# Performance work log

Hardware: AMD Instinct MI355X
Metric: run time of the kernel (lower is better)

Reference implementation:

```python
import jax, jax.numpy as jnp
import numpy as np

N_NODES = 100000
N_EDGES = 3200000
IN_CH = 32
HID = 16


def setup_inputs() -> dict:
    key = jax.random.key(0)
    ks = jax.random.split(key, 8)
    x = jax.random.normal(ks[0], (N_NODES, IN_CH), dtype=jnp.float32)
    edge_index = jax.random.randint(ks[1], (2, N_EDGES), 0, N_NODES, dtype=jnp.int64)
    s1 = 1.0 / np.sqrt(IN_CH)
    s2 = 1.0 / np.sqrt(HID)
    Wl1 = jax.random.normal(ks[2], (HID, IN_CH), dtype=jnp.float32) * s1
    Wr1 = jax.random.normal(ks[3], (HID, IN_CH), dtype=jnp.float32) * s1
    b1 = jnp.zeros((HID,), dtype=jnp.float32)
    Wl2 = jax.random.normal(ks[4], (1, HID), dtype=jnp.float32) * s2
    Wr2 = jax.random.normal(ks[5], (1, HID), dtype=jnp.float32) * s2
    b2 = jnp.zeros((1,), dtype=jnp.float32)
    return {"x": x, "edge_index": edge_index, "Wl1": Wl1, "Wr1": Wr1,
            "b1": b1, "Wl2": Wl2, "Wr2": Wr2, "b2": b2}


def _sage_conv(h, src, dst, deg_inv, Wl, Wr, b):
    # mean aggregation of source features at destination nodes
    msg_sum = jax.ops.segment_sum(h[src], dst, num_segments=N_NODES)  # [N, F]
    agg = msg_sum * deg_inv[:, None]
    # lin_l(agg) + lin_r(h): lin_l carries the bias (PyG SAGEConv convention)
    return agg @ Wl.T + b + h @ Wr.T


def reference(x, edge_index, Wl1, Wr1, b1, Wl2, Wr2, b2):
    src = edge_index[0]
    dst = edge_index[1]
    deg = jax.ops.segment_sum(jnp.ones((N_EDGES,), dtype=x.dtype), dst,
                              num_segments=N_NODES)
    deg_inv = 1.0 / jnp.maximum(deg, 1.0)  # mean; nodes w/o in-edges get 0 agg

    h = _sage_conv(x, src, dst, deg_inv, Wl1, Wr1, b1)
    h = jax.nn.relu(h)
    # F.dropout in eval mode -> identity
    out = _sage_conv(h, src, dst, deg_inv, Wl2, Wr2, b2)
    return out.squeeze(-1)  # [N]
```

## Files before the change

kernel.cpp:

```cpp
#include <hip/hip_runtime.h>

#define N_NODES 100000
#define N_EDGES 3200000
#define NB_F 782
#define RSZ 4992
#define TILE 6250
#define NTILES 512
#define PRJ_BLOCKS 196
#define MAXIT 13
#define MAXB 10


__device__ __forceinline__ float bf2f_lo(unsigned int w) {
  return __uint_as_float(w << 16);
}
__device__ __forceinline__ float bf2f_hi(unsigned int w) {
  return __uint_as_float(w & 0xFFFF0000u);
}
__device__ __forceinline__ unsigned short f2bf(float f) {
  unsigned int b = __float_as_uint(f);
  return (unsigned short)((b + 0x7FFFu + ((b >> 16) & 1u)) >> 16);
}

__global__ __launch_bounds__(512) void k_front(
    const int* __restrict__ ei, const float* __restrict__ x,
    const float* __restrict__ Wl1, const float* __restrict__ Wr1,
    const float* __restrict__ b1, int* __restrict__ gcur,
    int* __restrict__ recs, unsigned short* __restrict__ p1h,
    float* __restrict__ q1b) {
  __shared__ int smem[11693];
  const int t = threadIdx.x;

  if (blockIdx.x < PRJ_BLOCKS) {
    float* sWl = (float*)smem;
    float* sWr = (float*)smem + 512;
    float* sb  = (float*)smem + 1024;
    sWl[t] = Wl1[t];
    sWr[t] = Wr1[t];
    if (t < 16) sb[t] = b1[t];
    __syncthreads();

    const int n = blockIdx.x * 512 + t;
    if (n >= N_NODES) return;

    float xr[32];
    const float4* xp = (const float4*)(x + (size_t)n * 32);
#pragma unroll
    for (int j = 0; j < 8; ++j) {
      float4 v = xp[j];
      xr[4 * j + 0] = v.x;
      xr[4 * j + 1] = v.y;
      xr[4 * j + 2] = v.z;
      xr[4 * j + 3] = v.w;
    }
    float pv[16], qv[16];
#pragma unroll
    for (int hh = 0; hh < 16; ++hh) {
      float a = 0.f, b = 0.f;
#pragma unroll
      for (int i = 0; i < 32; ++i) {
        a = fmaf(xr[i], sWl[hh * 32 + i], a);
        b = fmaf(xr[i], sWr[hh * 32 + i], b);
      }
      pv[hh] = a;
      qv[hh] = b + sb[hh];
    }
    unsigned int w[8];
#pragma unroll
    for (int j = 0; j < 8; ++j)
      w[j] = (unsigned int)f2bf(pv[2 * j]) |
             ((unsigned int)f2bf(pv[2 * j + 1]) << 16);
    uint4* pp = (uint4*)(p1h + (size_t)n * 16);
    pp[0] = make_uint4(w[0], w[1], w[2], w[3]);
    pp[1] = make_uint4(w[4], w[5], w[6], w[7]);
    float4* qp = (float4*)(q1b + (size_t)n * 16);
#pragma unroll
    for (int j = 0; j < 4; ++j)
      qp[j] =
          make_float4(qv[4 * j], qv[4 * j + 1], qv[4 * j + 2], qv[4 * j + 3]);
    return;
  }

  int* hist   = smem;
  int* delta  = smem + 1024;
  int* seg    = smem + 1806;
  int* stage  = smem + 2318;
  unsigned short* bid = (unsigned short*)(smem + 8568);
  for (int i = t; i < 1024; i += 512) hist[i] = 0;
  __syncthreads();

  const int tb = (blockIdx.x - PRJ_BLOCKS) * TILE;
  int rec[MAXIT], aux[MAXIT];
#pragma unroll
  for (int i = 0; i < MAXIT; ++i) {
    const int pos = t + i * 512;
    if (pos < TILE) {
      const int e = tb + pos;
      const int s = ei[e];
      const int d = ei[N_EDGES + e];
      const int k = d >> 7;
      const int rank = atomicAdd(&hist[k], 1);
      rec[i] = ((d & 127) << 17) | s;
      aux[i] = (k << 16) | rank;
    } else {
      aux[i] = -1;
    }
  }
  __syncthreads();

  const int s0 = hist[2 * t], s1 = hist[2 * t + 1];
  const int my = s0 + s1;
  seg[t] = my;
  __syncthreads();
#pragma unroll
  for (int o = 1; o < 512; o <<= 1) {
    const int a = (t >= o) ? seg[t - o] : 0;
    __syncthreads();
    seg[t] += a;
    __syncthreads();
  }
  const int ex = seg[t] - my;
  hist[2 * t] = ex;
  hist[2 * t + 1] = ex + s0;
  {
    const int b = 2 * t;
    if (b < NB_F && s0)
      delta[b] = b * RSZ + atomicAdd(&gcur[b * 16], s0) - ex;
    if (b + 1 < NB_F && s1)
      delta[b + 1] =
          (b + 1) * RSZ + atomicAdd(&gcur[(b + 1) * 16], s1) - (ex + s0);
  }
  __syncthreads();

#pragma unroll
  for (int i = 0; i < MAXIT; ++i) {
    if (aux[i] >= 0) {
      const int k = aux[i] >> 16;
      const int rank = aux[i] & 0xFFFF;
      stage[hist[k] + rank] = rec[i];
    }
  }
  for (int k2 = t; k2 < NB_F; k2 += 512) {
    const int st = hist[k2];
    const int en = hist[k2 + 1];
    for (int p = st; p < en; ++p) bid[p] = (unsigned short)k2;
  }
  __syncthreads();

  for (int pos = t; pos < TILE; pos += 512) {
    const int k = bid[pos];
    const int idx = delta[k] + pos;
    if ((unsigned)idx < (unsigned)(NB_F * RSZ)) recs[idx] = stage[pos];
  }
}

__global__ __launch_bounds__(512) void k_sortagg1(
    const int* __restrict__ gcur, int* __restrict__ recs,
    const unsigned short* __restrict__ p1h, const float* __restrict__ q1b,
    const float* __restrict__ Wl2, const float* __restrict__ Wr2,
    float* __restrict__ p2, float* __restrict__ r2,
    float* __restrict__ deg_inv, int* __restrict__ node_off,
    int* __restrict__ node_cnt) {
  __shared__ int hist[128];
  __shared__ int nstart[128];
  __shared__ int ssort[RSZ];
  __shared__ float sWl[16], sWr[16];
  const int t = threadIdx.x;
  const int kb = blockIdx.x;
  const int b0 = kb * RSZ;
  const int gend = b0 + gcur[kb * 16];
  if (t < 128) hist[t] = 0;
  if (t < 16) {
    sWl[t] = Wl2[t];
    sWr[t] = Wr2[t];
  }
  __syncthreads();

  int rc[MAXB], ax[MAXB];
#pragma unroll
  for (int i = 0; i < MAXB; ++i) {
    const int r = b0 + t + i * 512;
    if (r < gend) {
      const int rec = recs[r];
      const int local = rec >> 17;
      const int rank = atomicAdd(&hist[local], 1);
      rc[i] = rec & 0x1FFFF;
      ax[i] = (local << 13) | rank;
    } else {
      ax[i] = -1;
    }
  }
  __syncthreads();

  {
    int v = (t < 128) ? hist[t] : 0;
    if (t < 128) nstart[t] = v;
    __syncthreads();
#pragma unroll
    for (int o = 1; o < 128; o <<= 1) {
      const int a = (t < 128 && t >= o) ? nstart[t - o] : 0;
      __syncthreads();
      if (t < 128) nstart[t] += a;
      __syncthreads();
    }
    if (t < 128) nstart[t] -= v;
  }
  __syncthreads();

#pragma unroll
  for (int i = 0; i < MAXB; ++i) {
    if (ax[i] >= 0) ssort[nstart[ax[i] >> 13] + (ax[i] & 0x1FFF)] = rc[i];
  }
  __syncthreads();

  const int T = gend - b0;
  for (int j2 = t; j2 < T; j2 += 512) recs[b0 + j2] = ssort[j2];
  if (t < 128) {
    node_off[kb * 128 + t] = b0 + nstart[t];
    node_cnt[kb * 128 + t] = hist[t];
  }

  const int local = t >> 2;
  const int quad = t & 3;
  const int half = quad & 1;
  const int epar = quad >> 1;
  const int n = kb * 128 + local;
  if (n >= N_NODES) return;
  const int st = nstart[local];
  const int k = hist[local];
  const unsigned short* pb = p1h + half * 8;

  float acc[8];
#pragma unroll
  for (int i = 0; i < 8; ++i) acc[i] = 0.f;
  int j = epar;
  for (; j + 6 < k; j += 8) {
    const int s0 = ssort[st + j], s1 = ssort[st + j + 2],
              s2 = ssort[st + j + 4], s3 = ssort[st + j + 6];
    const uint4 w0 = *(const uint4*)(pb + (size_t)s0 * 16);
    const uint4 w1 = *(const uint4*)(pb + (size_t)s1 * 16);
    const uint4 w2 = *(const uint4*)(pb + (size_t)s2 * 16);
    const uint4 w3 = *(const uint4*)(pb + (size_t)s3 * 16);
    acc[0] += (bf2f_lo(w0.x) + bf2f_lo(w1.x)) + (bf2f_lo(w2.x) + bf2f_lo(w3.x));
    acc[1] += (bf2f_hi(w0.x) + bf2f_hi(w1.x)) + (bf2f_hi(w2.x) + bf2f_hi(w3.x));
    acc[2] += (bf2f_lo(w0.y) + bf2f_lo(w1.y)) + (bf2f_lo(w2.y) + bf2f_lo(w3.y));
    acc[3] += (bf2f_hi(w0.y) + bf2f_hi(w1.y)) + (bf2f_hi(w2.y) + bf2f_hi(w3.y));
    acc[4] += (bf2f_lo(w0.z) + bf2f_lo(w1.z)) + (bf2f_lo(w2.z) + bf2f_lo(w3.z));
    acc[5] += (bf2f_hi(w0.z) + bf2f_hi(w1.z)) + (bf2f_hi(w2.z) + bf2f_hi(w3.z));
    acc[6] += (bf2f_lo(w0.w) + bf2f_lo(w1.w)) + (bf2f_lo(w2.w) + bf2f_lo(w3.w));
    acc[7] += (bf2f_hi(w0.w) + bf2f_hi(w1.w)) + (bf2f_hi(w2.w) + bf2f_hi(w3.w));
  }
  for (; j < k; j += 2) {
    const uint4 w = *(const uint4*)(pb + (size_t)ssort[st + j] * 16);
    acc[0] += bf2f_lo(w.x);
    acc[1] += bf2f_hi(w.x);
    acc[2] += bf2f_lo(w.y);
    acc[3] += bf2f_hi(w.y);
    acc[4] += bf2f_lo(w.z);
    acc[5] += bf2f_hi(w.z);
    acc[6] += bf2f_lo(w.w);
    acc[7] += bf2f_hi(w.w);
  }
#pragma unroll
  for (int i = 0; i < 8; ++i) acc[i] += __shfl_xor(acc[i], 2);

  const float di = 1.f / fmaxf((float)k, 1.f);
  const float4* qp = (const float4*)(q1b + (size_t)n * 16 + half * 8);
  const float4 qa = qp[0], qb = qp[1];
  float h[8];
  h[0] = fmaxf(fmaf(acc[0], di, qa.x), 0.f);
  h[1] = fmaxf(fmaf(acc[1], di, qa.y), 0.f);
  h[2] = fmaxf(fmaf(acc[2], di, qa.z), 0.f);
  h[3] = fmaxf(fmaf(acc[3], di, qa.w), 0.f);
  h[4] = fmaxf(fmaf(acc[4], di, qb.x), 0.f);
  h[5] = fmaxf(fmaf(acc[5], di, qb.y), 0.f);
  h[6] = fmaxf(fmaf(acc[6], di, qb.z), 0.f);
  h[7] = fmaxf(fmaf(acc[7], di, qb.w), 0.f);
  float pa = 0.f, pbv = 0.f;
#pragma unroll
  for (int i = 0; i < 8; ++i) {
    pa = fmaf(h[i], sWl[half * 8 + i], pa);
    pbv = fmaf(h[i], sWr[half * 8 + i], pbv);
  }
  pa += __shfl_xor(pa, 1);
  pbv += __shfl_xor(pbv, 1);
  if (quad == 0) {
    p2[n] = pa;
    r2[n] = pbv;
    deg_inv[n] = di;
  }
}

__global__ __launch_bounds__(512) void k_agg2out(
    const int* __restrict__ node_off, const int* __restrict__ node_cnt,
    const int* __restrict__ recs, const float* __restrict__ p2,
    const float* __restrict__ r2, const float* __restrict__ deg_inv,
    const float* __restrict__ b2, float* __restrict__ out) {
  const int t = threadIdx.x;
  const int n = blockIdx.x * 128 + (t >> 2);
  const int c = t & 3;
  if (n >= N_NODES) return;
  const int k0 = node_off[n];
  const int k = node_cnt[n];
  const int* sl = recs + k0;

  float u = 0.f;
  int j = c;
  for (; j + 4 < k; j += 8) u += p2[sl[j]] + p2[sl[j + 4]];
  for (; j < k; j += 4) u += p2[sl[j]];
  u += __shfl_xor(u, 1);
  u += __shfl_xor(u, 2);
  if (c == 0) out[n] = fmaf(u, deg_inv[n], r2[n] + b2[0]);
}

extern "C" void kernel_launch(void* const* d_in, const int* in_sizes, int n_in,
                              void* d_out, int out_size, void* d_ws,
                              size_t ws_size, hipStream_t stream) {
  const float* x   = (const float*)d_in[0];
  const int*   ei  = (const int*)d_in[1];
  const float* Wl1 = (const float*)d_in[2];
  const float* Wr1 = (const float*)d_in[3];
  const float* b1  = (const float*)d_in[4];
  const float* Wl2 = (const float*)d_in[5];
  const float* Wr2 = (const float*)d_in[6];
  const float* b2  = (const float*)d_in[7];
  float* out = (float*)d_out;

  const size_t N = N_NODES;
  int* wi = (int*)d_ws;
  int* gcur     = wi;
  int* node_off = wi + NB_F * 16;
  int* node_cnt = node_off + NB_F * 128;
  int* recs     = node_cnt + NB_F * 128;
  unsigned short* p1h = (unsigned short*)(recs + (size_t)NB_F * RSZ);
  float* q1b     = (float*)(p1h + 16 * N);
  float* p2      = q1b + 16 * N;
  float* r2      = p2 + N;
  float* deg_inv = r2 + N;

  hipMemsetAsync(gcur, 0, NB_F * 16 * sizeof(int), stream);
  k_front<<<PRJ_BLOCKS + NTILES, 512, 0, stream>>>(ei, x, Wl1, Wr1, b1, gcur,
                                                   recs, p1h, q1b);
  k_sortagg1<<<NB_F, 512, 0, stream>>>(gcur, recs, p1h, q1b, Wl2, Wr2, p2, r2,
                                       deg_inv, node_off, node_cnt);
  k_agg2out<<<NB_F, 512, 0, stream>>>(node_off, node_cnt, recs, p2, r2,
                                      deg_inv, b2, out);
}
```

Before: 177.7 us.

## Fold projection into sort-tile blocks and rebucket nodes into 768 buckets of 131

```diff
diff --git a/kernel.cpp b/kernel.cpp
--- a/kernel.cpp
+++ b/kernel.cpp
@@ -2,11 +2,12 @@
 
 #define N_NODES 100000
 #define N_EDGES 3200000
-#define NB_F 782
-#define RSZ 4992
+#define NB 768
+#define BKN 131
+#define RSZ 5120
 #define TILE 6250
 #define NTILES 512
-#define PRJ_BLOCKS 196
+#define PRJ_PER_BLOCK 196
 #define MAXIT 13
 #define MAXB 10
 
@@ -28,10 +29,10 @@
     const float* __restrict__ b1, int* __restrict__ gcur,
     int* __restrict__ recs, unsigned short* __restrict__ p1h,
     float* __restrict__ q1b) {
-  __shared__ int smem[11693];
+  __shared__ int smem[11679];
   const int t = threadIdx.x;
 
-  if (blockIdx.x < PRJ_BLOCKS) {
+  {
     float* sWl = (float*)smem;
     float* sWr = (float*)smem + 512;
     float* sb  = (float*)smem + 1024;
@@ -40,56 +41,56 @@
     if (t < 16) sb[t] = b1[t];
     __syncthreads();
 
-    const int n = blockIdx.x * 512 + t;
-    if (n >= N_NODES) return;
-
-    float xr[32];
-    const float4* xp = (const float4*)(x + (size_t)n * 32);
-#pragma unroll
-    for (int j = 0; j < 8; ++j) {
-      float4 v = xp[j];
-      xr[4 * j + 0] = v.x;
-      xr[4 * j + 1] = v.y;
-      xr[4 * j + 2] = v.z;
-      xr[4 * j + 3] = v.w;
-    }
-    float pv[16], qv[16];
-#pragma unroll
-    for (int hh = 0; hh < 16; ++hh) {
-      float a = 0.f, b = 0.f;
-#pragma unroll
-      for (int i = 0; i < 32; ++i) {
-        a = fmaf(xr[i], sWl[hh * 32 + i], a);
-        b = fmaf(xr[i], sWr[hh * 32 + i], b);
+    const int n = blockIdx.x * PRJ_PER_BLOCK + t;
+    if (t < PRJ_PER_BLOCK && n < N_NODES) {
+      float xr[32];
+      const float4* xp = (const float4*)(x + (size_t)n * 32);
+#pragma unroll
+      for (int j = 0; j < 8; ++j) {
+        float4 v = xp[j];
+        xr[4 * j + 0] = v.x;
+        xr[4 * j + 1] = v.y;
+        xr[4 * j + 2] = v.z;
+        xr[4 * j + 3] = v.w;
       }
-      pv[hh] = a;
-      qv[hh] = b + sb[hh];
-    }
-    unsigned int w[8];
-#pragma unroll
-    for (int j = 0; j < 8; ++j)
-      w[j] = (unsigned int)f2bf(pv[2 * j]) |
-             ((unsigned int)f2bf(pv[2 * j + 1]) << 16);
-    uint4* pp = (uint4*)(p1h + (size_t)n * 16);
-    pp[0] = make_uint4(w[0], w[1], w[2], w[3]);
-    pp[1] = make_uint4(w[4], w[5], w[6], w[7]);
-    float4* qp = (float4*)(q1b + (size_t)n * 16);
-#pragma unroll
-    for (int j = 0; j < 4; ++j)
-      qp[j] =
-          make_float4(qv[4 * j], qv[4 * j + 1], qv[4 * j + 2], qv[4 * j + 3]);
-    return;
+      float pv[16], qv[16];
+#pragma unroll
+      for (int hh = 0; hh < 16; ++hh) {
+        float a = 0.f, b = 0.f;
+#pragma unroll
+        for (int i = 0; i < 32; ++i) {
+          a = fmaf(xr[i], sWl[hh * 32 + i], a);
+          b = fmaf(xr[i], sWr[hh * 32 + i], b);
+        }
+        pv[hh] = a;
+        qv[hh] = b + sb[hh];
+      }
+      unsigned int w[8];
+#pragma unroll
+      for (int j = 0; j < 8; ++j)
+        w[j] = (unsigned int)f2bf(pv[2 * j]) |
+               ((unsigned int)f2bf(pv[2 * j + 1]) << 16);
+      uint4* pp = (uint4*)(p1h + (size_t)n * 16);
+      pp[0] = make_uint4(w[0], w[1], w[2], w[3]);
+      pp[1] = make_uint4(w[4], w[5], w[6], w[7]);
+      float4* qp = (float4*)(q1b + (size_t)n * 16);
+#pragma unroll
+      for (int j = 0; j < 4; ++j)
+        qp[j] =
+            make_float4(qv[4 * j], qv[4 * j + 1], qv[4 * j + 2], qv[4 * j + 3]);
+    }
+    __syncthreads();
   }
 
   int* hist   = smem;
   int* delta  = smem + 1024;
-  int* seg    = smem + 1806;
-  int* stage  = smem + 2318;
-  unsigned short* bid = (unsigned short*)(smem + 8568);
+  int* seg    = smem + 1792;
+  int* stage  = smem + 2304;
+  unsigned short* bid = (unsigned short*)(smem + 8554);
   for (int i = t; i < 1024; i += 512) hist[i] = 0;
   __syncthreads();
 
-  const int tb = (blockIdx.x - PRJ_BLOCKS) * TILE;
+  const int tb = blockIdx.x * TILE;
   int rec[MAXIT], aux[MAXIT];
 #pragma unroll
   for (int i = 0; i < MAXIT; ++i) {
@@ -98,9 +99,9 @@
       const int e = tb + pos;
       const int s = ei[e];
       const int d = ei[N_EDGES + e];
-      const int k = d >> 7;
+      const int k = (int)((unsigned)d / 131u);
       const int rank = atomicAdd(&hist[k], 1);
-      rec[i] = ((d & 127) << 17) | s;
+      rec[i] = ((d - k * 131) << 17) | s;
       aux[i] = (k << 16) | rank;
     } else {
       aux[i] = -1;
@@ -124,9 +125,8 @@
   hist[2 * t + 1] = ex + s0;
   {
     const int b = 2 * t;
-    if (b < NB_F && s0)
-      delta[b] = b * RSZ + atomicAdd(&gcur[b * 16], s0) - ex;
-    if (b + 1 < NB_F && s1)
+    if (b < NB && s0) delta[b] = b * RSZ + atomicAdd(&gcur[b * 16], s0) - ex;
+    if (b + 1 < NB && s1)
       delta[b + 1] =
           (b + 1) * RSZ + atomicAdd(&gcur[(b + 1) * 16], s1) - (ex + s0);
   }
@@ -136,11 +136,10 @@
   for (int i = 0; i < MAXIT; ++i) {
     if (aux[i] >= 0) {
       const int k = aux[i] >> 16;
-      const int rank = aux[i] & 0xFFFF;
-      stage[hist[k] + rank] = rec[i];
-    }
-  }
-  for (int k2 = t; k2 < NB_F; k2 += 512) {
+      stage[hist[k] + (aux[i] & 0xFFFF)] = rec[i];
+    }
+  }
+  for (int k2 = t; k2 < NB; k2 += 512) {
     const int st = hist[k2];
     const int en = hist[k2 + 1];
     for (int p = st; p < en; ++p) bid[p] = (unsigned short)k2;
@@ -150,7 +149,7 @@
   for (int pos = t; pos < TILE; pos += 512) {
     const int k = bid[pos];
     const int idx = delta[k] + pos;
-    if ((unsigned)idx < (unsigned)(NB_F * RSZ)) recs[idx] = stage[pos];
+    if ((unsigned)idx < (unsigned)(NB * RSZ)) recs[idx] = stage[pos];
   }
 }
 
@@ -161,15 +160,15 @@
     float* __restrict__ p2, float* __restrict__ r2,
     float* __restrict__ deg_inv, int* __restrict__ node_off,
     int* __restrict__ node_cnt) {
-  __shared__ int hist[128];
-  __shared__ int nstart[128];
+  __shared__ int hist[132];
+  __shared__ int nstart[132];
   __shared__ int ssort[RSZ];
   __shared__ float sWl[16], sWr[16];
   const int t = threadIdx.x;
   const int kb = blockIdx.x;
   const int b0 = kb * RSZ;
   const int gend = b0 + gcur[kb * 16];
-  if (t < 128) hist[t] = 0;
+  if (t < 132) hist[t] = 0;
   if (t < 16) {
     sWl[t] = Wl2[t];
     sWr[t] = Wr2[t];
@@ -193,17 +192,17 @@
   __syncthreads();
 
   {
-    int v = (t < 128) ? hist[t] : 0;
-    if (t < 128) nstart[t] = v;
-    __syncthreads();
-#pragma unroll
-    for (int o = 1; o < 128; o <<= 1) {
-      const int a = (t < 128 && t >= o) ? nstart[t - o] : 0;
+    int v = (t < 132) ? hist[t] : 0;
+    if (t < 132) nstart[t] = v;
+    __syncthreads();
+#pragma unroll
+    for (int o = 1; o < 132; o <<= 1) {
+      const int a = (t < 132 && t >= o) ? nstart[t - o] : 0;
       __syncthreads();
-      if (t < 128) nstart[t] += a;
+      if (t < 132) nstart[t] += a;
       __syncthreads();
     }
-    if (t < 128) nstart[t] -= v;
+    if (t < 132) nstart[t] -= v;
   }
   __syncthreads();
 
@@ -215,79 +214,92 @@
 
   const int T = gend - b0;
   for (int j2 = t; j2 < T; j2 += 512) recs[b0 + j2] = ssort[j2];
-  if (t < 128) {
-    node_off[kb * 128 + t] = b0 + nstart[t];
-    node_cnt[kb * 128 + t] = hist[t];
-  }
-
-  const int local = t >> 2;
+  if (t < BKN) {
+    const int n2 = kb * BKN + t;
+    node_off[n2] = b0 + nstart[t];
+    node_cnt[n2] = hist[t];
+  }
+
   const int quad = t & 3;
   const int half = quad & 1;
   const int epar = quad >> 1;
-  const int n = kb * 128 + local;
-  if (n >= N_NODES) return;
-  const int st = nstart[local];
-  const int k = hist[local];
   const unsigned short* pb = p1h + half * 8;
-
-  float acc[8];
-#pragma unroll
-  for (int i = 0; i < 8; ++i) acc[i] = 0.f;
-  int j = epar;
-  for (; j + 6 < k; j += 8) {
-    const int s0 = ssort[st + j], s1 = ssort[st + j + 2],
-              s2 = ssort[st + j + 4], s3 = ssort[st + j + 6];
-    const uint4 w0 = *(const uint4*)(pb + (size_t)s0 * 16);
-    const uint4 w1 = *(const uint4*)(pb + (size_t)s1 * 16);
-    const uint4 w2 = *(const uint4*)(pb + (size_t)s2 * 16);
-    const uint4 w3 = *(const uint4*)(pb + (size_t)s3 * 16);
-    acc[0] += (bf2f_lo(w0.x) + bf2f_lo(w1.x)) + (bf2f_lo(w2.x) + bf2f_lo(w3.x));
-    acc[1] += (bf2f_hi(w0.x) + bf2f_hi(w1.x)) + (bf2f_hi(w2.x) + bf2f_hi(w3.x));
-    acc[2] += (bf2f_lo(w0.y) + bf2f_lo(w1.y)) + (bf2f_lo(w2.y) + bf2f_lo(w3.y));
-    acc[3] += (bf2f_hi(w0.y) + bf2f_hi(w1.y)) + (bf2f_hi(w2.y) + bf2f_hi(w3.y));
-    acc[4] += (bf2f_lo(w0.z) + bf2f_lo(w1.z)) + (bf2f_lo(w2.z) + bf2f_lo(w3.z));
-    acc[5] += (bf2f_hi(w0.z) + bf2f_hi(w1.z)) + (bf2f_hi(w2.z) + bf2f_hi(w3.z));
-    acc[6] += (bf2f_lo(w0.w) + bf2f_lo(w1.w)) + (bf2f_lo(w2.w) + bf2f_lo(w3.w));
-    acc[7] += (bf2f_hi(w0.w) + bf2f_hi(w1.w)) + (bf2f_hi(w2.w) + bf2f_hi(w3.w));
-  }
-  for (; j < k; j += 2) {
-    const uint4 w = *(const uint4*)(pb + (size_t)ssort[st + j] * 16);
-    acc[0] += bf2f_lo(w.x);
-    acc[1] += bf2f_hi(w.x);
-    acc[2] += bf2f_lo(w.y);
-    acc[3] += bf2f_hi(w.y);
-    acc[4] += bf2f_lo(w.z);
-    acc[5] += bf2f_hi(w.z);
-    acc[6] += bf2f_lo(w.w);
-    acc[7] += bf2f_hi(w.w);
-  }
-#pragma unroll
-  for (int i = 0; i < 8; ++i) acc[i] += __shfl_xor(acc[i], 2);
-
-  const float di = 1.f / fmaxf((float)k, 1.f);
-  const float4* qp = (const float4*)(q1b + (size_t)n * 16 + half * 8);
-  const float4 qa = qp[0], qb = qp[1];
-  float h[8];
-  h[0] = fmaxf(fmaf(acc[0], di, qa.x), 0.f);
-  h[1] = fmaxf(fmaf(acc[1], di, qa.y), 0.f);
-  h[2] = fmaxf(fmaf(acc[2], di, qa.z), 0.f);
-  h[3] = fmaxf(fmaf(acc[3], di, qa.w), 0.f);
-  h[4] = fmaxf(fmaf(acc[4], di, qb.x), 0.f);
-  h[5] = fmaxf(fmaf(acc[5], di, qb.y), 0.f);
-  h[6] = fmaxf(fmaf(acc[6], di, qb.z), 0.f);
-  h[7] = fmaxf(fmaf(acc[7], di, qb.w), 0.f);
-  float pa = 0.f, pbv = 0.f;
-#pragma unroll
-  for (int i = 0; i < 8; ++i) {
-    pa = fmaf(h[i], sWl[half * 8 + i], pa);
-    pbv = fmaf(h[i], sWr[half * 8 + i], pbv);
-  }
-  pa += __shfl_xor(pa, 1);
-  pbv += __shfl_xor(pbv, 1);
-  if (quad == 0) {
-    p2[n] = pa;
-    r2[n] = pbv;
-    deg_inv[n] = di;
+#pragma unroll
+  for (int p = 0; p < 2; ++p) {
+    const int local = p * 128 + (t >> 2);
+    if (local >= BKN) continue;
+    const int n = kb * BKN + local;
+    if (n >= N_NODES) continue;
+    const int st = nstart[local];
+    const int k = hist[local];
+
+    float acc[8];
+#pragma unroll
+    for (int i = 0; i < 8; ++i) acc[i] = 0.f;
+    int j = epar;
+    for (; j + 6 < k; j += 8) {
+      const int s0 = ssort[st + j], s1 = ssort[st + j + 2],
+                s2 = ssort[st + j + 4], s3 = ssort[st + j + 6];
+      const uint4 w0 = *(const uint4*)(pb + (size_t)s0 * 16);
+      const uint4 w1 = *(const uint4*)(pb + (size_t)s1 * 16);
+      const uint4 w2 = *(const uint4*)(pb + (size_t)s2 * 16);
+      const uint4 w3 = *(const uint4*)(pb + (size_t)s3 * 16);
+      acc[0] +=
+          (bf2f_lo(w0.x) + bf2f_lo(w1.x)) + (bf2f_lo(w2.x) + bf2f_lo(w3.x));
+      acc[1] +=
+          (bf2f_hi(w0.x) + bf2f_hi(w1.x)) + (bf2f_hi(w2.x) + bf2f_hi(w3.x));
+      acc[2] +=
+          (bf2f_lo(w0.y) + bf2f_lo(w1.y)) + (bf2f_lo(w2.y) + bf2f_lo(w3.y));
+      acc[3] +=
+          (bf2f_hi(w0.y) + bf2f_hi(w1.y)) + (bf2f_hi(w2.y) + bf2f_hi(w3.y));
+      acc[4] +=
+          (bf2f_lo(w0.z) + bf2f_lo(w1.z)) + (bf2f_lo(w2.z) + bf2f_lo(w3.z));
+      acc[5] +=
+          (bf2f_hi(w0.z) + bf2f_hi(w1.z)) + (bf2f_hi(w2.z) + bf2f_hi(w3.z));
+      acc[6] +=
+          (bf2f_lo(w0.w) + bf2f_lo(w1.w)) + (bf2f_lo(w2.w) + bf2f_lo(w3.w));
+      acc[7] +=
+          (bf2f_hi(w0.w) + bf2f_hi(w1.w)) + (bf2f_hi(w2.w) + bf2f_hi(w3.w));
+    }
+    for (; j < k; j += 2) {
+      const uint4 w = *(const uint4*)(pb + (size_t)ssort[st + j] * 16);
+      acc[0] += bf2f_lo(w.x);
+      acc[1] += bf2f_hi(w.x);
+      acc[2] += bf2f_lo(w.y);
+      acc[3] += bf2f_hi(w.y);
+      acc[4] += bf2f_lo(w.z);
+      acc[5] += bf2f_hi(w.z);
+      acc[6] += bf2f_lo(w.w);
+      acc[7] += bf2f_hi(w.w);
+    }
+#pragma unroll
+    for (int i = 0; i < 8; ++i) acc[i] += __shfl_xor(acc[i], 2);
+
+    const float di = 1.f / fmaxf((float)k, 1.f);
+    const float4* qp = (const float4*)(q1b + (size_t)n * 16 + half * 8);
+    const float4 qa = qp[0], qb = qp[1];
+    float h[8];
+    h[0] = fmaxf(fmaf(acc[0], di, qa.x), 0.f);
+    h[1] = fmaxf(fmaf(acc[1], di, qa.y), 0.f);
+    h[2] = fmaxf(fmaf(acc[2], di, qa.z), 0.f);
+    h[3] = fmaxf(fmaf(acc[3], di, qa.w), 0.f);
+    h[4] = fmaxf(fmaf(acc[4], di, qb.x), 0.f);
+    h[5] = fmaxf(fmaf(acc[5], di, qb.y), 0.f);
+    h[6] = fmaxf(fmaf(acc[6], di, qb.z), 0.f);
+    h[7] = fmaxf(fmaf(acc[7], di, qb.w), 0.f);
+    float pa = 0.f, pbv = 0.f;
+#pragma unroll
+    for (int i = 0; i < 8; ++i) {
+      pa = fmaf(h[i], sWl[half * 8 + i], pa);
+      pbv = fmaf(h[i], sWr[half * 8 + i], pbv);
+    }
+    pa += __shfl_xor(pa, 1);
+    pbv += __shfl_xor(pbv, 1);
+    if (quad == 0) {
+      p2[n] = pa;
+      r2[n] = pbv;
+      deg_inv[n] = di;
+    }
   }
 }
 
@@ -329,20 +341,20 @@
   const size_t N = N_NODES;
   int* wi = (int*)d_ws;
   int* gcur     = wi;
-  int* node_off = wi + NB_F * 16;
-  int* node_cnt = node_off + NB_F * 128;
-  int* recs     = node_cnt + NB_F * 128;
-  unsigned short* p1h = (unsigned short*)(recs + (size_t)NB_F * RSZ);
+  int* node_off = wi + NB * 16;
+  int* node_cnt = node_off + 100608;
+  int* recs     = node_cnt + 100608;
+  unsigned short* p1h = (unsigned short*)(recs + (size_t)NB * RSZ);
   float* q1b     = (float*)(p1h + 16 * N);
   float* p2      = q1b + 16 * N;
   float* r2      = p2 + N;
   float* deg_inv = r2 + N;
 
-  hipMemsetAsync(gcur, 0, NB_F * 16 * sizeof(int), stream);
-  k_front<<<PRJ_BLOCKS + NTILES, 512, 0, stream>>>(ei, x, Wl1, Wr1, b1, gcur,
-                                                   recs, p1h, q1b);
-  k_sortagg1<<<NB_F, 512, 0, stream>>>(gcur, recs, p1h, q1b, Wl2, Wr2, p2, r2,
-                                       deg_inv, node_off, node_cnt);
-  k_agg2out<<<NB_F, 512, 0, stream>>>(node_off, node_cnt, recs, p2, r2,
-                                      deg_inv, b2, out);
-}
+  hipMemsetAsync(gcur, 0, NB * 16 * sizeof(int), stream);
+  k_front<<<NTILES, 512, 0, stream>>>(ei, x, Wl1, Wr1, b1, gcur, recs, p1h,
+                                      q1b);
+  k_sortagg1<<<NB, 512, 0, stream>>>(gcur, recs, p1h, q1b, Wl2, Wr2, p2, r2,
+                                     deg_inv, node_off, node_cnt);
+  k_agg2out<<<(N_NODES + 127) / 128, 512, 0, stream>>>(
+      node_off, node_cnt, recs, p2, r2, deg_inv, b2, out);
+}
```

New measurement: 184.9 us. 4.1% more time.
